# Kernel optimization log

Hardware: AMD Instinct MI355X
Metric: run time of the kernel (lower is better)

Reference implementation:

```python
import jax, jax.numpy as jnp
import numpy as np

K_SIZE = 2
STRIDE = 2
PAD = 0
EPS = 1e-8


def setup_inputs() -> dict:
    key = jax.random.key(0)
    # (batch, quat_groups, 4, H, W)
    x = jax.random.normal(key, (8, 64, 4, 128, 128), dtype=jnp.float32)
    return {"x": x}


def _unfold(x, k, s, p):
    """Replicates F.unfold patch extraction on (B,G,4,H,W).
    Returns (B, G, 4, k*k, L) with unfold's (kernel-row, kernel-col) ordering,
    plus H_out, W_out."""
    B, G, Q, H, W = x.shape
    xp = jnp.pad(x, ((0, 0), (0, 0), (0, 0), (p, p), (p, p)))
    Ho = (H + 2 * p - k) // s + 1
    Wo = (W + 2 * p - k) // s + 1
    patches = []
    for i in range(k):          # fixed small kernel loop (k*k = 4)
        for j in range(k):
            patches.append(xp[:, :, :, i:i + s * Ho:s, j:j + s * Wo:s])
    u = jnp.stack(patches, axis=3)            # (B,G,4,k*k,Ho,Wo)
    return u.reshape(B, G, Q, k * k, Ho * Wo), Ho, Wo


def reference(x):
    B, G, Q, H, W = x.shape
    u, Ho, Wo = _unfold(x, K_SIZE, STRIDE, PAD)     # (B,G,4,K,L)
    # per-window quaternion magnitude
    mag = jnp.sqrt(jnp.sum(u * u, axis=2))          # (B,G,K,L)
    # NOTE: faithful to source — normalization is over the L (output-position)
    # axis (dim=3), entropy summed over kernel-area axis (dim=2)
    p = mag / (jnp.sum(mag, axis=3, keepdims=True) + EPS)
    ent = -jnp.sum(p * jnp.log(p + EPS), axis=2)    # (B,G,L)
    idx = jnp.argmax(ent, axis=1)                   # (B,L), first max like torch
    # gather max-entropy quaternion group per output position
    sel = jnp.take_along_axis(u, idx[:, None, None, None, :], axis=1)[:, 0]  # (B,4,K,L)
    pooled = jnp.transpose(sel, (0, 3, 1, 2))       # (B,L,4,K) matches torch adv-index layout
    return pooled.reshape(B, -1, Ho, Wo)            # (B, 4*K, Ho, Wo), faithful quirky view
```

## Files before the change

kernel.cpp:

```cpp
#include <hip/hip_runtime.h>
#include <math.h>

#define NB 8
#define NG 64
#define NQ 4
#define NH 128
#define NW 128
#define NL 4096
#define EPSF 1e-8f

#define WINNER_CT (NB * NL)

__global__ __launch_bounds__(1024) void fused_kernel(const float4* __restrict__ x4,
                                                     unsigned long long* __restrict__ winner) {
    int bg = blockIdx.x;
    int b = bg >> 6;
    int g = bg & 63;
    int tid = threadIdx.x;

    long base4 = (long)(bg * NQ) * (NH * NW / 4);

    float mg[2][2][4];
    double dsum[4] = {0.0, 0.0, 0.0, 0.0};
#pragma unroll
    for (int pp = 0; pp < 2; pp++) {
        int pos = tid + pp * 1024;
        int ho = pos >> 5, wp = pos & 31;
        float sqA[4] = {0.f, 0.f, 0.f, 0.f};
        float sqB[4] = {0.f, 0.f, 0.f, 0.f};
#pragma unroll
        for (int q = 0; q < NQ; q++) {
#pragma unroll
            for (int i = 0; i < 2; i++) {
                float4 v = x4[base4 + (long)q * (NH * NW / 4) + (2 * ho + i) * (NW / 4) + wp];
                sqA[i * 2]     = __fadd_rn(sqA[i * 2],     __fmul_rn(v.x, v.x));
                sqA[i * 2 + 1] = __fadd_rn(sqA[i * 2 + 1], __fmul_rn(v.y, v.y));
                sqB[i * 2]     = __fadd_rn(sqB[i * 2],     __fmul_rn(v.z, v.z));
                sqB[i * 2 + 1] = __fadd_rn(sqB[i * 2 + 1], __fmul_rn(v.w, v.w));
            }
        }
#pragma unroll
        for (int k = 0; k < 4; k++) {
            float mA = __fsqrt_rn(sqA[k]);
            float mB = __fsqrt_rn(sqB[k]);
            mg[pp][0][k] = mA;
            mg[pp][1][k] = mB;
            dsum[k] += (double)mA + (double)mB;
        }
    }

#pragma unroll
    for (int k = 0; k < 4; k++) {
#pragma unroll
        for (int off = 32; off; off >>= 1) dsum[k] += __shfl_xor(dsum[k], off, 64);
    }
    __shared__ double lds[16][4];
    __shared__ float rcp4s[4];
    int wave = tid >> 6, lane = tid & 63;
    if (lane == 0) {
#pragma unroll
        for (int k = 0; k < 4; k++) lds[wave][k] = dsum[k];
    }
    __syncthreads();
    if (tid < 4) {
        double s = 0.0;
        for (int w = 0; w < 16; w++) s += lds[w][tid];
        float denom = __fadd_rn((float)s, EPSF);
        rcp4s[tid] = (float)(1.0 / (double)denom);
    }
    __syncthreads();
    float r0 = rcp4s[0], r1 = rcp4s[1], r2 = rcp4s[2], r3 = rcp4s[3];

    unsigned long long gk = (unsigned long long)(63 - g);
    unsigned long long* wrow = winner + b * NL;
#pragma unroll
    for (int pp = 0; pp < 2; pp++) {
        int pos = tid + pp * 1024;
        int ho = pos >> 5, wp = pos & 31;
#pragma unroll
        for (int w = 0; w < 2; w++) {
            float p0 = __fmul_rn(mg[pp][w][0], r0);
            float p1 = __fmul_rn(mg[pp][w][1], r1);
            float p2 = __fmul_rn(mg[pp][w][2], r2);
            float p3 = __fmul_rn(mg[pp][w][3], r3);
            float e = 0.f;
            e = __fadd_rn(e, __fmul_rn(p0, logf(__fadd_rn(p0, EPSF))));
            e = __fadd_rn(e, __fmul_rn(p1, logf(__fadd_rn(p1, EPSF))));
            e = __fadd_rn(e, __fmul_rn(p2, logf(__fadd_rn(p2, EPSF))));
            e = __fadd_rn(e, __fmul_rn(p3, logf(__fadd_rn(p3, EPSF))));
            float f = -e;
            unsigned int bits = __float_as_uint(f);
            unsigned int key = (bits & 0x80000000u) ? ~bits : (bits | 0x80000000u);
            int l = ho * 64 + 2 * wp + w;
            atomicMax(&wrow[l], ((unsigned long long)key << 32) | gk);
        }
    }
}

__global__ __launch_bounds__(256) void gather_kernel(const float2* __restrict__ x2,
                                                     const unsigned long long* __restrict__ winner,
                                                     float4* __restrict__ out4) {
    int t = blockIdx.x * 256 + threadIdx.x;
    int q = t & 3;
    int l = (t >> 2) & 4095;
    int b = t >> 14;
    unsigned long long w = winner[b * NL + l];
    int g = 63 - (int)(w & 63ull);
    int ho = l >> 6, wo = l & 63;
    long base2 = (long)((b * NG + g) * NQ + q) * (NH * NW / 2);
    float2 t0 = x2[base2 + (2 * ho) * (NW / 2) + wo];
    float2 t1 = x2[base2 + (2 * ho + 1) * (NW / 2) + wo];
    out4[t] = make_float4(t0.x, t0.y, t1.x, t1.y);
}

extern "C" void kernel_launch(void* const* d_in, const int* in_sizes, int n_in,
                              void* d_out, int out_size, void* d_ws, size_t ws_size,
                              hipStream_t stream) {
    const float* x = (const float*)d_in[0];
    float* out = (float*)d_out;
    unsigned long long* winner = (unsigned long long*)d_ws;

    hipMemsetAsync(winner, 0, (size_t)WINNER_CT * 8, stream);

    fused_kernel<<<NB * NG, 1024, 0, stream>>>((const float4*)x, winner);
    gather_kernel<<<(NB * NL * NQ) / 256, 256, 0, stream>>>(
        (const float2*)x, winner, (float4*)out);
}
```

Measured before the change: 209.8 us.

## Replace global 64-bit atomicMax with entropy buffer and argmax in gather kernel

The fused kernel now writes each group's sortable entropy key to a per-(b,g,l) buffer instead of doing a 64-bit atomicMax per output position. The gather kernel splits the 64 groups across the 4 quaternion lanes, takes 16 keys each, and combines them with two shuffles to find the first maximum before gathering. This removes the memset and contended atomics, at the cost of an extra 8 MB intermediate that is written and then read back.

```diff
diff --git a/kernel.cpp b/kernel.cpp
--- a/kernel.cpp
+++ b/kernel.cpp
@@ -9,13 +9,10 @@
 #define NL 4096
 #define EPSF 1e-8f
 
-#define WINNER_CT (NB * NL)
 
 __global__ __launch_bounds__(1024) void fused_kernel(const float4* __restrict__ x4,
-                                                     unsigned long long* __restrict__ winner) {
+                                                     unsigned int* __restrict__ ent) {
     int bg = blockIdx.x;
-    int b = bg >> 6;
-    int g = bg & 63;
     int tid = threadIdx.x;
 
     long base4 = (long)(bg * NQ) * (NH * NW / 4);
@@ -71,12 +68,12 @@
     __syncthreads();
     float r0 = rcp4s[0], r1 = rcp4s[1], r2 = rcp4s[2], r3 = rcp4s[3];
 
-    unsigned long long gk = (unsigned long long)(63 - g);
-    unsigned long long* wrow = winner + b * NL;
+    unsigned int* erow = ent + ((unsigned)bg << 12);
 #pragma unroll
     for (int pp = 0; pp < 2; pp++) {
         int pos = tid + pp * 1024;
         int ho = pos >> 5, wp = pos & 31;
+        unsigned int keys[2];
 #pragma unroll
         for (int w = 0; w < 2; w++) {
             float p0 = __fmul_rn(mg[pp][w][0], r0);
@@ -90,22 +87,39 @@
             e = __fadd_rn(e, __fmul_rn(p3, logf(__fadd_rn(p3, EPSF))));
             float f = -e;
             unsigned int bits = __float_as_uint(f);
-            unsigned int key = (bits & 0x80000000u) ? ~bits : (bits | 0x80000000u);
-            int l = ho * 64 + 2 * wp + w;
-            atomicMax(&wrow[l], ((unsigned long long)key << 32) | gk);
+            keys[w] = (bits & 0x80000000u) ? ~bits : (bits | 0x80000000u);
         }
+        int l0 = ho * 64 + 2 * wp;
+        *reinterpret_cast<uint2*>(erow + l0) = make_uint2(keys[0], keys[1]);
     }
 }
 
-__global__ __launch_bounds__(256) void gather_kernel(const float2* __restrict__ x2,
-                                                     const unsigned long long* __restrict__ winner,
-                                                     float4* __restrict__ out4) {
+__global__ __launch_bounds__(256) void argmax_gather_kernel(const float2* __restrict__ x2,
+                                                            const unsigned int* __restrict__ ent,
+                                                            float4* __restrict__ out4) {
     int t = blockIdx.x * 256 + threadIdx.x;
     int q = t & 3;
     int l = (t >> 2) & 4095;
     int b = t >> 14;
-    unsigned long long w = winner[b * NL + l];
-    int g = 63 - (int)(w & 63ull);
+
+    const unsigned int* eb = ent + ((unsigned)(b * NG + q * 16) << 12) + l;
+    unsigned long long best = 0ull;
+#pragma unroll
+    for (int i = 0; i < 16; i++) {
+        unsigned int key = eb[(long)i << 12];
+        int g = q * 16 + i;
+        unsigned long long cur =
+            ((unsigned long long)key << 32) | (unsigned long long)(63 - g);
+        if (cur > best) best = cur;
+    }
+    {
+        unsigned long long o1 = __shfl_xor(best, 1, 64);
+        if (o1 > best) best = o1;
+        unsigned long long o2 = __shfl_xor(best, 2, 64);
+        if (o2 > best) best = o2;
+    }
+    int g = 63 - (int)(best & 63ull);
+
     int ho = l >> 6, wo = l & 63;
     long base2 = (long)((b * NG + g) * NQ + q) * (NH * NW / 2);
     float2 t0 = x2[base2 + (2 * ho) * (NW / 2) + wo];
@@ -118,11 +132,9 @@
                               hipStream_t stream) {
     const float* x = (const float*)d_in[0];
     float* out = (float*)d_out;
-    unsigned long long* winner = (unsigned long long*)d_ws;
+    unsigned int* ent = (unsigned int*)d_ws;
 
-    hipMemsetAsync(winner, 0, (size_t)WINNER_CT * 8, stream);
-
-    fused_kernel<<<NB * NG, 1024, 0, stream>>>((const float4*)x, winner);
-    gather_kernel<<<(NB * NL * NQ) / 256, 256, 0, stream>>>(
-        (const float2*)x, winner, (float4*)out);
+    fused_kernel<<<NB * NG, 1024, 0, stream>>>((const float4*)x, ent);
+    argmax_gather_kernel<<<(NB * NL * NQ) / 256, 256, 0, stream>>>(
+        (const float2*)x, ent, (float4*)out);
 }
```

Result: faster. 198.1 us (-5.5%).
